# Performance work log

Hardware: AMD Instinct MI355X
Metric: run time of the kernel (lower is better)

## Reference

```python
import jax, jax.numpy as jnp
import numpy as np

SCALE_POS = 2.0
SCALE_NEG = 40.0
THRESH_POS = 0.5
THRESH_NEG = 0.5
MARGIN = 0.1
EPS = 1e-5


def setup_inputs() -> dict:
    key = jax.random.key(0)
    kf, kl = jax.random.split(key)
    B, D, NUM_CLASSES = 4096, 1024, 64
    feats = jax.random.normal(kf, (B, D), dtype=jnp.float32)
    feats = feats / jnp.linalg.norm(feats, axis=1, keepdims=True)  # L2-normalized embeddings
    labels = jax.random.randint(kl, (B,), 0, NUM_CLASSES, dtype=jnp.int64)
    return {"feats": feats, "labels": labels}


def reference(feats, labels):
    B = feats.shape[0]
    sim = jnp.matmul(feats, feats.T)  # [B, B]
    same = labels[:, None] == labels[None, :]
    pos_mask = same & (sim < 1.0 - EPS)  # drop self / near-duplicate pairs
    neg_mask = ~same

    # hard mining: keep negatives above min positive - margin, positives below max negative + margin
    min_pos = jnp.min(jnp.where(pos_mask, sim, jnp.inf), axis=1)   # [B]
    max_neg = jnp.max(jnp.where(neg_mask, sim, -jnp.inf), axis=1)  # [B]
    neg_sel = neg_mask & (sim + MARGIN > min_pos[:, None])
    pos_sel = pos_mask & (sim - MARGIN < max_neg[:, None])

    pos_sum = jnp.sum(jnp.where(pos_sel, jnp.exp(-SCALE_POS * (sim - THRESH_POS)), 0.0), axis=1)
    neg_sum = jnp.sum(jnp.where(neg_sel, jnp.exp(SCALE_NEG * (sim - THRESH_NEG)), 0.0), axis=1)
    pos_loss = jnp.log1p(pos_sum) / SCALE_POS
    neg_loss = jnp.log1p(neg_sum) / SCALE_NEG

    valid = jnp.any(pos_sel, axis=1) & jnp.any(neg_sel, axis=1)  # rows skipped by original loop
    return jnp.sum(jnp.where(valid, pos_loss + neg_loss, 0.0)) / B
```

## Files before the change

kernel.cpp:

```cpp
#include <hip/hip_runtime.h>

typedef _Float16 half8 __attribute__((ext_vector_type(8)));
typedef float floatx4 __attribute__((ext_vector_type(4)));
typedef int intx4 __attribute__((ext_vector_type(4)));
typedef int intx8 __attribute__((ext_vector_type(8)));
typedef __attribute__((address_space(1))) const void gvoid;
typedef __attribute__((address_space(3))) void svoid;

#define SCALE_POS 2.0f
#define SCALE_NEG 40.0f
#define THRESH 0.5f
#define MARGIN 0.1f
#define EPSV 1e-5f

__global__ void k_init(const float* __restrict__ feats,
                       unsigned char* __restrict__ f8,
                       float* __restrict__ out,
                       int total4) {
    int i = blockIdx.x * blockDim.x + threadIdx.x;
    if (i < total4) {
        float4 v = ((const float4*)feats)[i];
        int w = 0;
        w = __builtin_amdgcn_cvt_pk_fp8_f32(v.x, v.y, w, false);
        w = __builtin_amdgcn_cvt_pk_fp8_f32(v.z, v.w, w, true);
        ((int*)f8)[i] = w;
    }
    if (i == 0) out[0] = 0.f;
}

__global__ void __launch_bounds__(256, 4)
k_gemm_h(const unsigned char* __restrict__ f8,
         const int* __restrict__ labels,
         float* __restrict__ pmin,
         float* __restrict__ pmax,
         _Float16* __restrict__ simh,
         int D, int nb) {
    __shared__ __align__(16) unsigned char As[128 * 128];
    __shared__ __align__(16) unsigned char Bs[128 * 128];
    __shared__ int labR[128], labC[128];

    const int Bsz = nb * 128;

    const int bid0 = blockIdx.x;
    const int t = (bid0 & 7) * 66 + (bid0 >> 3);
    int rb = 0, rem = t;
    while (rem >= nb - rb) { rem -= nb - rb; ++rb; }
    const int cb = rb + rem;
    const int rowBase = rb * 128;
    const int colBase = cb * 128;

    const int tid = threadIdx.x;
    const int lane = tid & 63;
    const int wave = tid >> 6;
    const int wr = wave >> 1;
    const int wc = wave & 1;
    const int q = lane >> 4;
    const int cIn = lane & 15;

    if (tid < 128) labR[tid] = labels[rowBase + tid];
    else           labC[tid - 128] = labels[colBase + (tid - 128)];

    const int subrow = lane >> 3;
    const int swz = (lane & 7) ^ subrow;
    const unsigned char* gP[8];
    unsigned char* lP[8];
#pragma unroll
    for (int j = 0; j < 8; ++j) {
        const int c = wave * 8 + j;
        const int grow = (c < 16) ? (rowBase + c * 8 + subrow)
                                  : (colBase + (c - 16) * 8 + subrow);
        gP[j] = f8 + (size_t)grow * D + swz * 16;
        lP[j] = ((c < 16) ? (As + c * 1024) : (Bs + (c - 16) * 1024)) + lane * 16;
    }

    int aOff0[4], aOff1[4], bOff0[4], bOff1[4];
#pragma unroll
    for (int i = 0; i < 4; ++i) {
        const int rA = wr * 64 + i * 16 + cIn;
        aOff0[i] = rA * 128 + ((2 * q) ^ (rA & 7)) * 16;
        aOff1[i] = rA * 128 + ((2 * q + 1) ^ (rA & 7)) * 16;
        const int rB = wc * 64 + i * 16 + cIn;
        bOff0[i] = rB * 128 + ((2 * q) ^ (rB & 7)) * 16;
        bOff1[i] = rB * 128 + ((2 * q + 1) ^ (rB & 7)) * 16;
    }

    floatx4 acc[4][4] = {};

    const int KT = D >> 7;
    for (int kt = 0; kt < KT; ++kt) {
        const int kOff = kt * 128;
        __syncthreads();
#pragma unroll
        for (int j = 0; j < 8; ++j)
            __builtin_amdgcn_global_load_lds((gvoid*)(gP[j] + kOff), (svoid*)lP[j], 16, 0, 0);
        __syncthreads();

        intx8 a[4], b[4];
#pragma unroll
        for (int i = 0; i < 4; ++i) {
            intx4 lo = *(const intx4*)(As + aOff0[i]);
            intx4 hi = *(const intx4*)(As + aOff1[i]);
            a[i] = __builtin_shufflevector(lo, hi, 0, 1, 2, 3, 4, 5, 6, 7);
        }
#pragma unroll
        for (int i = 0; i < 4; ++i) {
            intx4 lo = *(const intx4*)(Bs + bOff0[i]);
            intx4 hi = *(const intx4*)(Bs + bOff1[i]);
            b[i] = __builtin_shufflevector(lo, hi, 0, 1, 2, 3, 4, 5, 6, 7);
        }
#pragma unroll
        for (int i = 0; i < 4; ++i)
#pragma unroll
            for (int j2 = 0; j2 < 4; ++j2)
                acc[i][j2] = __builtin_amdgcn_mfma_scale_f32_16x16x128_f8f6f4(
                    a[i], b[j2], acc[i][j2], 0, 0,
                    0, 0x7f7f7f7f,
                    0, 0x7f7f7f7f);
    }

    int rLabv[16];
#pragma unroll
    for (int mi = 0; mi < 4; ++mi)
#pragma unroll
        for (int rr = 0; rr < 4; ++rr)
            rLabv[mi * 4 + rr] = labR[wr * 64 + mi * 16 + q * 4 + rr];
    int cLabv[4];
#pragma unroll
    for (int ni = 0; ni < 4; ++ni)
        cLabv[ni] = labC[wc * 64 + ni * 16 + cIn];

    {
        half8* dst = (half8*)(simh + (size_t)(2 * t + wc) * 8192
                                   + (size_t)(wr * 64 + lane) * 64);
#pragma unroll
        for (int mi = 0; mi < 4; ++mi) {
            half8 h0, h1;
#pragma unroll
            for (int ni = 0; ni < 2; ++ni)
#pragma unroll
                for (int rr = 0; rr < 4; ++rr) {
                    h0[ni * 4 + rr] = (_Float16)acc[mi][ni][rr];
                    h1[ni * 4 + rr] = (_Float16)acc[mi][ni + 2][rr];
                }
            dst[mi * 2] = h0;
            dst[mi * 2 + 1] = h1;
        }
    }

    {
        float* pmnRow = pmin + (size_t)(2 * cb + wc) * Bsz + rowBase;
        float* pmxRow = pmax + (size_t)(2 * cb + wc) * Bsz + rowBase;
#pragma unroll
        for (int mi = 0; mi < 4; ++mi)
#pragma unroll
            for (int rr = 0; rr < 4; ++rr) {
                const int rLoc = wr * 64 + mi * 16 + q * 4 + rr;
                const int rLab = rLabv[mi * 4 + rr];
                float vmin = 1e30f, vmax = -1e30f;
#pragma unroll
                for (int ni = 0; ni < 4; ++ni) {
                    float s = acc[mi][ni][rr];
                    if (rLab == cLabv[ni]) {
                        if (s < 1.0f - EPSV) vmin = fminf(vmin, s);
                    } else {
                        vmax = fmaxf(vmax, s);
                    }
                }
#pragma unroll
                for (int off = 8; off; off >>= 1) {
                    vmin = fminf(vmin, __shfl_xor(vmin, off, 16));
                    vmax = fmaxf(vmax, __shfl_xor(vmax, off, 16));
                }
                if (cIn == 0) {
                    pmnRow[rLoc] = vmin;
                    pmxRow[rLoc] = vmax;
                }
            }
    }

    if (rb != cb) {
        float* pmnCol = pmin + (size_t)(2 * rb + wr) * Bsz + colBase;
        float* pmxCol = pmax + (size_t)(2 * rb + wr) * Bsz + colBase;
#pragma unroll
        for (int ni = 0; ni < 4; ++ni) {
            const int cLab = cLabv[ni];
            float vmin = 1e30f, vmax = -1e30f;
#pragma unroll
            for (int mi = 0; mi < 4; ++mi)
#pragma unroll
                for (int rr = 0; rr < 4; ++rr) {
                    float s = acc[mi][ni][rr];
                    if (rLabv[mi * 4 + rr] == cLab) {
                        if (s < 1.0f - EPSV) vmin = fminf(vmin, s);
                    } else {
                        vmax = fmaxf(vmax, s);
                    }
                }
            vmin = fminf(vmin, __shfl_xor(vmin, 16, 64));
            vmin = fminf(vmin, __shfl_xor(vmin, 32, 64));
            vmax = fmaxf(vmax, __shfl_xor(vmax, 16, 64));
            vmax = fmaxf(vmax, __shfl_xor(vmax, 32, 64));
            if (q == 0) {
                const int cLoc = wc * 64 + ni * 16 + cIn;
                pmnCol[cLoc] = vmin;
                pmxCol[cLoc] = vmax;
            }
        }
    }
}

__global__ void __launch_bounds__(256)
k_stats(const float* __restrict__ pmin, const float* __restrict__ pmax,
        float* __restrict__ gateN, float* __restrict__ gateP, int B) {
    const int r = blockIdx.x * 256 + threadIdx.x;
    float mn = 1e30f, mx = -1e30f;
    for (int k = 0; k < 64; ++k) {
        mn = fminf(mn, pmin[(size_t)k * B + r]);
        mx = fmaxf(mx, pmax[(size_t)k * B + r]);
    }
    gateN[r] = mn - MARGIN;
    gateP[r] = mx + MARGIN;
}

__global__ void __launch_bounds__(256)
k_sum2f(const _Float16* __restrict__ simh,
        const int* __restrict__ labels,
        const float* __restrict__ gateN,
        const float* __restrict__ gateP,
        float* __restrict__ psP, float* __restrict__ psN,
        int nb, int B) {
    __shared__ int labR[128], labC[128];
    __shared__ float gNR[128], gPR[128], gNC[128], gPC[128];

    int t = blockIdx.x;
    int rb = 0, rem = t;
    while (rem >= nb - rb) { rem -= nb - rb; ++rb; }
    const int cb = rb + rem;
    const int rowBase = rb * 128;

    const int tid = threadIdx.x;
    const int sub = tid >> 7;
    const int stid = tid & 127;
    const int wave = stid >> 6;
    const int lane = tid & 63;
    const int q = lane >> 4;
    const int cIn = lane & 15;
    const int colBase = cb * 128 + sub * 64;

    if (tid < 128) {
        labR[tid] = labels[rowBase + tid];
        gNR[tid] = gateN[rowBase + tid];
        gPR[tid] = gateP[rowBase + tid];
    } else {
        const int j = tid - 128;
        labC[j] = labels[cb * 128 + j];
        gNC[j] = gateN[cb * 128 + j];
        gPC[j] = gateP[cb * 128 + j];
    }
    __syncthreads();

    int cLabv[4];
    float gNCv[4], gPCv[4];
#pragma unroll
    for (int ni = 0; ni < 4; ++ni) {
        const int j = sub * 64 + ni * 16 + cIn;
        cLabv[ni] = labC[j];
        gNCv[ni] = gNC[j];
        gPCv[ni] = gPC[j];
    }

    const half8* src = (const half8*)(simh + (size_t)(2 * t + sub) * 8192 + (size_t)stid * 64);
    half8 hv[8];
#pragma unroll
    for (int v = 0; v < 8; ++v) hv[v] = src[v];

    float cps[4] = {}, cns[4] = {};
    const bool offd = (rb != cb);

    float* psPRow = psP + (size_t)(2 * cb + sub) * B + rowBase;
    float* psNRow = psN + (size_t)(2 * cb + sub) * B + rowBase;

#pragma unroll
    for (int mi = 0; mi < 4; ++mi)
#pragma unroll
        for (int rr = 0; rr < 4; ++rr) {
            const int rLoc = wave * 64 + mi * 16 + q * 4 + rr;
            const int rLab = labR[rLoc];
            const float gn = gNR[rLoc];
            const float gp = gPR[rLoc];
            float rp = 0.f, rn = 0.f;
#pragma unroll
            for (int ni = 0; ni < 4; ++ni) {
                const int idx = mi * 16 + ni * 4 + rr;
                const float s = (float)hv[idx >> 3][idx & 7];
                if (rLab == cLabv[ni]) {
                    if (s < 1.0f - EPSV) {
                        float ev = __expf(-SCALE_POS * (s - THRESH));
                        if (s < gp) rp += ev;
                        if (offd && s < gPCv[ni]) cps[ni] += ev;
                    }
                } else {
                    float ev = __expf(SCALE_NEG * (s - THRESH));
                    if (s > gn) rn += ev;
                    if (offd && s > gNCv[ni]) cns[ni] += ev;
                }
            }
#pragma unroll
            for (int off = 8; off; off >>= 1) {
                rp += __shfl_xor(rp, off, 16);
                rn += __shfl_xor(rn, off, 16);
            }
            if (cIn == 0) {
                psPRow[rLoc] = rp;
                psNRow[rLoc] = rn;
            }
        }
    if (offd) {
        float* psPCol = psP + (size_t)(2 * rb + wave) * B + colBase;
        float* psNCol = psN + (size_t)(2 * rb + wave) * B + colBase;
#pragma unroll
        for (int ni = 0; ni < 4; ++ni) {
            cps[ni] += __shfl_xor(cps[ni], 16, 64);
            cps[ni] += __shfl_xor(cps[ni], 32, 64);
            cns[ni] += __shfl_xor(cns[ni], 16, 64);
            cns[ni] += __shfl_xor(cns[ni], 32, 64);
            if (q == 0) {
                const int cLoc = ni * 16 + cIn;
                psPCol[cLoc] = cps[ni];
                psNCol[cLoc] = cns[ni];
            }
        }
    }
}

__global__ void __launch_bounds__(256)
k_final(const float* __restrict__ psP, const float* __restrict__ psN,
        float* __restrict__ out, int B) {
    __shared__ float red[4];
    const int r = blockIdx.x * 256 + threadIdx.x;
    float P = 0.f, N = 0.f;
    for (int k = 0; k < 64; ++k) {
        P += psP[(size_t)k * B + r];
        N += psN[(size_t)k * B + r];
    }
    float a = (P > 0.f && N > 0.f)
                  ? log1pf(P) * (1.0f / SCALE_POS) + log1pf(N) * (1.0f / SCALE_NEG)
                  : 0.f;
#pragma unroll
    for (int off = 32; off; off >>= 1) a += __shfl_down(a, off, 64);
    const int tid = threadIdx.x;
    if ((tid & 63) == 0) red[tid >> 6] = a;
    __syncthreads();
    if (tid == 0)
        atomicAdd(out, (red[0] + red[1] + red[2] + red[3]) / (float)B);
}

extern "C" void kernel_launch(void* const* d_in, const int* in_sizes, int n_in,
                              void* d_out, int out_size, void* d_ws, size_t ws_size,
                              hipStream_t stream) {
    const float* feats = (const float*)d_in[0];
    const int* labels = (const int*)d_in[1];
    const int B = in_sizes[1];
    const int D = in_sizes[0] / B;
    const int nb = B / 128;
    const int NT = nb * (nb + 1) / 2;
    const int total4 = B * D / 4;

    char* ws = (char*)d_ws;
    unsigned char* f8 = (unsigned char*)ws;
    size_t off = (size_t)B * D;
    float* pmin = (float*)(ws + off); off += (size_t)64 * B * 4;
    float* pmax = (float*)(ws + off); off += (size_t)64 * B * 4;
    float* psP  = (float*)(ws + off); off += (size_t)64 * B * 4;
    float* psN  = (float*)(ws + off); off += (size_t)64 * B * 4;
    float* gateN = (float*)(ws + off); off += (size_t)B * 4;
    float* gateP = (float*)(ws + off); off += (size_t)B * 4;
    _Float16* simh = (_Float16*)(ws + ((off + 255) & ~(size_t)255));
    float* outp = (float*)d_out;

    k_init<<<(total4 + 255) / 256, 256, 0, stream>>>(feats, f8, outp, total4);

    k_gemm_h<<<NT, 256, 0, stream>>>(f8, labels, pmin, pmax, simh, D, nb);

    k_stats<<<B / 256, 256, 0, stream>>>(pmin, pmax, gateN, gateP, B);

    k_sum2f<<<NT, 256, 0, stream>>>(simh, labels, gateN, gateP, psP, psN, nb, B);

    k_final<<<B / 256, 256, 0, stream>>>(psP, psN, outp, B);
}
```

Measured before the change: 134.7 us.

## Register-prefetch next K tile while computing current tile in fp8 GEMM

Replaces direct global-to-LDS loads with a register-staged pipeline. The next K slice is loaded into registers while MFMAs run on the current LDS tile, then written to LDS after a barrier. This is meant to hide global load latency behind compute. It costs 32 extra VGPRs per thread for the staging buffer, so the launch-bounds occupancy hint drops from 4 to 2 blocks.

New measurement: 136.9 us. About the same (+1.6%).

```diff
diff --git a/kernel.cpp b/kernel.cpp
--- a/kernel.cpp
+++ b/kernel.cpp
@@ -4,8 +4,6 @@
 typedef float floatx4 __attribute__((ext_vector_type(4)));
 typedef int intx4 __attribute__((ext_vector_type(4)));
 typedef int intx8 __attribute__((ext_vector_type(8)));
-typedef __attribute__((address_space(1))) const void gvoid;
-typedef __attribute__((address_space(3))) void svoid;
 
 #define SCALE_POS 2.0f
 #define SCALE_NEG 40.0f
@@ -28,15 +26,14 @@
     if (i == 0) out[0] = 0.f;
 }
 
-__global__ void __launch_bounds__(256, 4)
+__global__ void __launch_bounds__(256, 2)
 k_gemm_h(const unsigned char* __restrict__ f8,
          const int* __restrict__ labels,
          float* __restrict__ pmin,
          float* __restrict__ pmax,
          _Float16* __restrict__ simh,
          int D, int nb) {
-    __shared__ __align__(16) unsigned char As[128 * 128];
-    __shared__ __align__(16) unsigned char Bs[128 * 128];
+    __shared__ __align__(16) unsigned char S[32 * 1024];
     __shared__ int labR[128], labC[128];
 
     const int Bsz = nb * 128;
@@ -61,16 +58,16 @@
     else           labC[tid - 128] = labels[colBase + (tid - 128)];
 
     const int subrow = lane >> 3;
-    const int swz = (lane & 7) ^ subrow;
-    const unsigned char* gP[8];
-    unsigned char* lP[8];
+    const int blk = lane & 7;
+    const unsigned char* gA[8];
+    int wOff[8];
 #pragma unroll
     for (int j = 0; j < 8; ++j) {
         const int c = wave * 8 + j;
         const int grow = (c < 16) ? (rowBase + c * 8 + subrow)
                                   : (colBase + (c - 16) * 8 + subrow);
-        gP[j] = f8 + (size_t)grow * D + swz * 16;
-        lP[j] = ((c < 16) ? (As + c * 1024) : (Bs + (c - 16) * 1024)) + lane * 16;
+        gA[j] = f8 + (size_t)grow * D + blk * 16;
+        wOff[j] = c * 1024 + subrow * 128 + ((blk ^ subrow) << 4);
     }
 
     int aOff0[4], aOff1[4], bOff0[4], bOff1[4];
@@ -80,43 +77,71 @@
         aOff0[i] = rA * 128 + ((2 * q) ^ (rA & 7)) * 16;
         aOff1[i] = rA * 128 + ((2 * q + 1) ^ (rA & 7)) * 16;
         const int rB = wc * 64 + i * 16 + cIn;
-        bOff0[i] = rB * 128 + ((2 * q) ^ (rB & 7)) * 16;
-        bOff1[i] = rB * 128 + ((2 * q + 1) ^ (rB & 7)) * 16;
+        bOff0[i] = 16384 + rB * 128 + ((2 * q) ^ (rB & 7)) * 16;
+        bOff1[i] = 16384 + rB * 128 + ((2 * q + 1) ^ (rB & 7)) * 16;
     }
 
     floatx4 acc[4][4] = {};
+    intx4 rg[8];
+
+#define LOADR(kt)                                                              \
+    {                                                                          \
+        _Pragma("unroll")                                                      \
+        for (int j = 0; j < 8; ++j)                                            \
+            rg[j] = *(const intx4*)(gA[j] + ((kt) << 7));                      \
+    }
+
+#define DSWRITE()                                                              \
+    {                                                                          \
+        _Pragma("unroll")                                                      \
+        for (int j = 0; j < 8; ++j)                                            \
+            *(intx4*)(S + wOff[j]) = rg[j];                                    \
+    }
+
+#define COMPUTE()                                                              \
+    {                                                                          \
+        intx8 a[4], b[4];                                                      \
+        _Pragma("unroll")                                                      \
+        for (int i = 0; i < 4; ++i) {                                          \
+            intx4 lo = *(const intx4*)(S + aOff0[i]);                          \
+            intx4 hi = *(const intx4*)(S + aOff1[i]);                          \
+            a[i] = __builtin_shufflevector(lo, hi, 0, 1, 2, 3, 4, 5, 6, 7);    \
+        }                                                                      \
+        _Pragma("unroll")                                                      \
+        for (int i = 0; i < 4; ++i) {                                          \
+            intx4 lo = *(const intx4*)(S + bOff0[i]);                          \
+            intx4 hi = *(const intx4*)(S + bOff1[i]);                          \
+            b[i] = __builtin_shufflevector(lo, hi, 0, 1, 2, 3, 4, 5, 6, 7);    \
+        }                                                                      \
+        _Pragma("unroll")                                                      \
+        for (int i = 0; i < 4; ++i)                                            \
+            _Pragma("unroll")                                                  \
+            for (int j2 = 0; j2 < 4; ++j2)                                     \
+                acc[i][j2] = __builtin_amdgcn_mfma_scale_f32_16x16x128_f8f6f4( \
+                    a[i], b[j2], acc[i][j2], 0, 0,                             \
+                    0, 0x7f7f7f7f, 0, 0x7f7f7f7f);                             \
+    }
 
     const int KT = D >> 7;
+
+    LOADR(0);
+    DSWRITE();
+
     for (int kt = 0; kt < KT; ++kt) {
-        const int kOff = kt * 128;
-        __syncthreads();
-#pragma unroll
-        for (int j = 0; j < 8; ++j)
-            __builtin_amdgcn_global_load_lds((gvoid*)(gP[j] + kOff), (svoid*)lP[j], 16, 0, 0);
-        __syncthreads();
-
-        intx8 a[4], b[4];
-#pragma unroll
-        for (int i = 0; i < 4; ++i) {
-            intx4 lo = *(const intx4*)(As + aOff0[i]);
-            intx4 hi = *(const intx4*)(As + aOff1[i]);
-            a[i] = __builtin_shufflevector(lo, hi, 0, 1, 2, 3, 4, 5, 6, 7);
+        if (kt + 1 < KT) LOADR(kt + 1);
+        asm volatile("s_waitcnt lgkmcnt(0)" ::: "memory");
+        __builtin_amdgcn_sched_barrier(0);
+        __builtin_amdgcn_s_barrier();
+        COMPUTE();
+        if (kt + 1 < KT) {
+            __syncthreads();
+            DSWRITE();
         }
-#pragma unroll
-        for (int i = 0; i < 4; ++i) {
-            intx4 lo = *(const intx4*)(Bs + bOff0[i]);
-            intx4 hi = *(const intx4*)(Bs + bOff1[i]);
-            b[i] = __builtin_shufflevector(lo, hi, 0, 1, 2, 3, 4, 5, 6, 7);
-        }
-#pragma unroll
-        for (int i = 0; i < 4; ++i)
-#pragma unroll
-            for (int j2 = 0; j2 < 4; ++j2)
-                acc[i][j2] = __builtin_amdgcn_mfma_scale_f32_16x16x128_f8f6f4(
-                    a[i], b[j2], acc[i][j2], 0, 0,
-                    0, 0x7f7f7f7f,
-                    0, 0x7f7f7f7f);
-    }
+    }
+
+#undef LOADR
+#undef DSWRITE
+#undef COMPUTE
 
     int rLabv[16];
 #pragma unroll
```

## Fuse GEMM, stats and exp-sum into one kernel with a grid barrier

Applied to the files above, without the earlier changes.

Merges the GEMM, row-stat reduction and masked exp-sum kernels into a single kernel. A global atomic counter serves as a grid-wide barrier, so each block keeps its similarity tile in registers instead of writing an fp16 copy and reading it back. After the barrier, each block recomputes the gates for its own rows and columns from the partial min/max buffers. This removes the fp16 similarity round trip through memory, two kernel launches and the precision loss of fp16 storage. It relies on all 528 blocks being resident at once, since the spin barrier would deadlock otherwise, and the occupancy hint is lowered from 4 to 3 blocks per CU.

After: 160.1 us. 1.19x slower.

```diff
diff --git a/kernel.cpp b/kernel.cpp
--- a/kernel.cpp
+++ b/kernel.cpp
@@ -1,6 +1,5 @@
 #include <hip/hip_runtime.h>
 
-typedef _Float16 half8 __attribute__((ext_vector_type(8)));
 typedef float floatx4 __attribute__((ext_vector_type(4)));
 typedef int intx4 __attribute__((ext_vector_type(4)));
 typedef int intx8 __attribute__((ext_vector_type(8)));
@@ -16,6 +15,7 @@
 __global__ void k_init(const float* __restrict__ feats,
                        unsigned char* __restrict__ f8,
                        float* __restrict__ out,
+                       unsigned* __restrict__ cnt,
                        int total4) {
     int i = blockIdx.x * blockDim.x + threadIdx.x;
     if (i < total4) {
@@ -25,19 +25,22 @@
         w = __builtin_amdgcn_cvt_pk_fp8_f32(v.z, v.w, w, true);
         ((int*)f8)[i] = w;
     }
-    if (i == 0) out[0] = 0.f;
+    if (i == 0) { out[0] = 0.f; cnt[0] = 0u; }
 }
 
-__global__ void __launch_bounds__(256, 4)
-k_gemm_h(const unsigned char* __restrict__ f8,
-         const int* __restrict__ labels,
-         float* __restrict__ pmin,
-         float* __restrict__ pmax,
-         _Float16* __restrict__ simh,
-         int D, int nb) {
+__global__ void __launch_bounds__(256, 3)
+k_fused(const unsigned char* __restrict__ f8,
+        const int* __restrict__ labels,
+        float* __restrict__ pmin,
+        float* __restrict__ pmax,
+        float* __restrict__ psP,
+        float* __restrict__ psN,
+        unsigned* __restrict__ cnt,
+        int D, int nb, int NTtot) {
     __shared__ __align__(16) unsigned char As[128 * 128];
     __shared__ __align__(16) unsigned char Bs[128 * 128];
     __shared__ int labR[128], labC[128];
+    __shared__ float gNR[128], gPR[128], gNC[128], gPC[128];
 
     const int Bsz = nb * 128;
 
@@ -129,23 +132,7 @@
     for (int ni = 0; ni < 4; ++ni)
         cLabv[ni] = labC[wc * 64 + ni * 16 + cIn];
 
-    {
-        half8* dst = (half8*)(simh + (size_t)(2 * t + wc) * 8192
-                                   + (size_t)(wr * 64 + lane) * 64);
-#pragma unroll
-        for (int mi = 0; mi < 4; ++mi) {
-            half8 h0, h1;
-#pragma unroll
-            for (int ni = 0; ni < 2; ++ni)
-#pragma unroll
-                for (int rr = 0; rr < 4; ++rr) {
-                    h0[ni * 4 + rr] = (_Float16)acc[mi][ni][rr];
-                    h1[ni * 4 + rr] = (_Float16)acc[mi][ni + 2][rr];
-                }
-            dst[mi * 2] = h0;
-            dst[mi * 2 + 1] = h1;
-        }
-    }
+    const bool offd = (rb != cb);
 
     {
         float* pmnRow = pmin + (size_t)(2 * cb + wc) * Bsz + rowBase;
@@ -177,8 +164,7 @@
                 }
             }
     }
-
-    if (rb != cb) {
+    if (offd) {
         float* pmnCol = pmin + (size_t)(2 * rb + wr) * Bsz + colBase;
         float* pmxCol = pmax + (size_t)(2 * rb + wr) * Bsz + colBase;
 #pragma unroll
@@ -207,127 +193,88 @@
             }
         }
     }
-}
-
-__global__ void __launch_bounds__(256)
-k_stats(const float* __restrict__ pmin, const float* __restrict__ pmax,
-        float* __restrict__ gateN, float* __restrict__ gateP, int B) {
-    const int r = blockIdx.x * 256 + threadIdx.x;
-    float mn = 1e30f, mx = -1e30f;
-    for (int k = 0; k < 64; ++k) {
-        mn = fminf(mn, pmin[(size_t)k * B + r]);
-        mx = fmaxf(mx, pmax[(size_t)k * B + r]);
-    }
-    gateN[r] = mn - MARGIN;
-    gateP[r] = mx + MARGIN;
-}
-
-__global__ void __launch_bounds__(256)
-k_sum2f(const _Float16* __restrict__ simh,
-        const int* __restrict__ labels,
-        const float* __restrict__ gateN,
-        const float* __restrict__ gateP,
-        float* __restrict__ psP, float* __restrict__ psN,
-        int nb, int B) {
-    __shared__ int labR[128], labC[128];
-    __shared__ float gNR[128], gPR[128], gNC[128], gPC[128];
-
-    int t = blockIdx.x;
-    int rb = 0, rem = t;
-    while (rem >= nb - rb) { rem -= nb - rb; ++rb; }
-    const int cb = rb + rem;
-    const int rowBase = rb * 128;
-
-    const int tid = threadIdx.x;
-    const int sub = tid >> 7;
-    const int stid = tid & 127;
-    const int wave = stid >> 6;
-    const int lane = tid & 63;
-    const int q = lane >> 4;
-    const int cIn = lane & 15;
-    const int colBase = cb * 128 + sub * 64;
-
-    if (tid < 128) {
-        labR[tid] = labels[rowBase + tid];
-        gNR[tid] = gateN[rowBase + tid];
-        gPR[tid] = gateP[rowBase + tid];
-    } else {
-        const int j = tid - 128;
-        labC[j] = labels[cb * 128 + j];
-        gNC[j] = gateN[cb * 128 + j];
-        gPC[j] = gateP[cb * 128 + j];
-    }
+
     __syncthreads();
-
-    int cLabv[4];
-    float gNCv[4], gPCv[4];
-#pragma unroll
-    for (int ni = 0; ni < 4; ++ni) {
-        const int j = sub * 64 + ni * 16 + cIn;
-        cLabv[ni] = labC[j];
-        gNCv[ni] = gNC[j];
-        gPCv[ni] = gPC[j];
-    }
-
-    const half8* src = (const half8*)(simh + (size_t)(2 * t + sub) * 8192 + (size_t)stid * 64);
-    half8 hv[8];
-#pragma unroll
-    for (int v = 0; v < 8; ++v) hv[v] = src[v];
-
-    float cps[4] = {}, cns[4] = {};
-    const bool offd = (rb != cb);
-
-    float* psPRow = psP + (size_t)(2 * cb + sub) * B + rowBase;
-    float* psNRow = psN + (size_t)(2 * cb + sub) * B + rowBase;
-
-#pragma unroll
-    for (int mi = 0; mi < 4; ++mi)
-#pragma unroll
-        for (int rr = 0; rr < 4; ++rr) {
-            const int rLoc = wave * 64 + mi * 16 + q * 4 + rr;
-            const int rLab = labR[rLoc];
-            const float gn = gNR[rLoc];
-            const float gp = gPR[rLoc];
-            float rp = 0.f, rn = 0.f;
+    if (tid == 0) {
+        __hip_atomic_fetch_add(cnt, 1u, __ATOMIC_RELEASE, __HIP_MEMORY_SCOPE_AGENT);
+        while (__hip_atomic_load(cnt, __ATOMIC_ACQUIRE, __HIP_MEMORY_SCOPE_AGENT)
+               < (unsigned)NTtot)
+            __builtin_amdgcn_s_sleep(2);
+    }
+    __syncthreads();
+
+    {
+        const int j = tid & 127;
+        const int base = (tid < 128) ? (rowBase + j) : (colBase + j);
+        float mn = 1e30f, mx = -1e30f;
+        for (int k = 0; k < 64; ++k) {
+            mn = fminf(mn, pmin[(size_t)k * Bsz + base]);
+            mx = fmaxf(mx, pmax[(size_t)k * Bsz + base]);
+        }
+        if (tid < 128) { gNR[j] = mn - MARGIN; gPR[j] = mx + MARGIN; }
+        else           { gNC[j] = mn - MARGIN; gPC[j] = mx + MARGIN; }
+    }
+    __syncthreads();
+
+    {
+        float gNCv[4], gPCv[4];
+#pragma unroll
+        for (int ni = 0; ni < 4; ++ni) {
+            const int j = wc * 64 + ni * 16 + cIn;
+            gNCv[ni] = gNC[j];
+            gPCv[ni] = gPC[j];
+        }
+        float cps[4] = {}, cns[4] = {};
+        float* psPRow = psP + (size_t)(2 * cb + wc) * Bsz + rowBase;
+        float* psNRow = psN + (size_t)(2 * cb + wc) * Bsz + rowBase;
+#pragma unroll
+        for (int mi = 0; mi < 4; ++mi)
+#pragma unroll
+            for (int rr = 0; rr < 4; ++rr) {
+                const int rLoc = wr * 64 + mi * 16 + q * 4 + rr;
+                const int rLab = rLabv[mi * 4 + rr];
+                const float gn = gNR[rLoc];
+                const float gp = gPR[rLoc];
+                float rp = 0.f, rn = 0.f;
+#pragma unroll
+                for (int ni = 0; ni < 4; ++ni) {
+                    const float s = acc[mi][ni][rr];
+                    if (rLab == cLabv[ni]) {
+                        if (s < 1.0f - EPSV) {
+                            float ev = __expf(-SCALE_POS * (s - THRESH));
+                            if (s < gp) rp += ev;
+                            if (offd && s < gPCv[ni]) cps[ni] += ev;
+                        }
+                    } else {
+                        float ev = __expf(SCALE_NEG * (s - THRESH));
+                        if (s > gn) rn += ev;
+                        if (offd && s > gNCv[ni]) cns[ni] += ev;
+                    }
+                }
+#pragma unroll
+                for (int off = 8; off; off >>= 1) {
+                    rp += __shfl_xor(rp, off, 16);
+                    rn += __shfl_xor(rn, off, 16);
+                }
+                if (cIn == 0) {
+                    psPRow[rLoc] = rp;
+                    psNRow[rLoc] = rn;
+                }
+            }
+        if (offd) {
+            float* psPCol = psP + (size_t)(2 * rb + wr) * Bsz + colBase;
+            float* psNCol = psN + (size_t)(2 * rb + wr) * Bsz + colBase;
 #pragma unroll
             for (int ni = 0; ni < 4; ++ni) {
-                const int idx = mi * 16 + ni * 4 + rr;
-                const float s = (float)hv[idx >> 3][idx & 7];
-                if (rLab == cLabv[ni]) {
-                    if (s < 1.0f - EPSV) {
-                        float ev = __expf(-SCALE_POS * (s - THRESH));
-                        if (s < gp) rp += ev;
-                        if (offd && s < gPCv[ni]) cps[ni] += ev;
-                    }
-                } else {
-                    float ev = __expf(SCALE_NEG * (s - THRESH));
-                    if (s > gn) rn += ev;
-                    if (offd && s > gNCv[ni]) cns[ni] += ev;
-                }
-            }
-#pragma unroll
-            for (int off = 8; off; off >>= 1) {
-                rp += __shfl_xor(rp, off, 16);
-                rn += __shfl_xor(rn, off, 16);
-            }
-            if (cIn == 0) {
-                psPRow[rLoc] = rp;
-                psNRow[rLoc] = rn;
-            }
-        }
-    if (offd) {
-        float* psPCol = psP + (size_t)(2 * rb + wave) * B + colBase;
-        float* psNCol = psN + (size_t)(2 * rb + wave) * B + colBase;
-#pragma unroll
-        for (int ni = 0; ni < 4; ++ni) {
-            cps[ni] += __shfl_xor(cps[ni], 16, 64);
-            cps[ni] += __shfl_xor(cps[ni], 32, 64);
-            cns[ni] += __shfl_xor(cns[ni], 16, 64);
-            cns[ni] += __shfl_xor(cns[ni], 32, 64);
-            if (q == 0) {
-                const int cLoc = ni * 16 + cIn;
-                psPCol[cLoc] = cps[ni];
-                psNCol[cLoc] = cns[ni];
+                cps[ni] += __shfl_xor(cps[ni], 16, 64);
+                cps[ni] += __shfl_xor(cps[ni], 32, 64);
+                cns[ni] += __shfl_xor(cns[ni], 16, 64);
+                cns[ni] += __shfl_xor(cns[ni], 32, 64);
+                if (q == 0) {
+                    const int cLoc = wc * 64 + ni * 16 + cIn;
+                    psPCol[cLoc] = cps[ni];
+                    psNCol[cLoc] = cns[ni];
+                }
             }
         }
     }
@@ -373,18 +320,12 @@
     float* pmax = (float*)(ws + off); off += (size_t)64 * B * 4;
     float* psP  = (float*)(ws + off); off += (size_t)64 * B * 4;
     float* psN  = (float*)(ws + off); off += (size_t)64 * B * 4;
-    float* gateN = (float*)(ws + off); off += (size_t)B * 4;
-    float* gateP = (float*)(ws + off); off += (size_t)B * 4;
-    _Float16* simh = (_Float16*)(ws + ((off + 255) & ~(size_t)255));
+    unsigned* cnt = (unsigned*)(ws + ((off + 255) & ~(size_t)255));
     float* outp = (float*)d_out;
 
-    k_init<<<(total4 + 255) / 256, 256, 0, stream>>>(feats, f8, outp, total4);
-
-    k_gemm_h<<<NT, 256, 0, stream>>>(f8, labels, pmin, pmax, simh, D, nb);
-
-    k_stats<<<B / 256, 256, 0, stream>>>(pmin, pmax, gateN, gateP, B);
-
-    k_sum2f<<<NT, 256, 0, stream>>>(simh, labels, gateN, gateP, psP, psN, nb, B);
+    k_init<<<(total4 + 255) / 256, 256, 0, stream>>>(feats, f8, outp, cnt, total4);
+
+    k_fused<<<NT, 256, 0, stream>>>(f8, labels, pmin, pmax, psP, psN, cnt, D, nb, NT);
 
     k_final<<<B / 256, 256, 0, stream>>>(psP, psN, outp, B);
 }
```
